# Performance work log

Hardware: AMD Instinct MI355X
Metric: run time of the kernel (lower is better)

The kernel has to match this reference:

```python
import jax, jax.numpy as jnp
import numpy as np

B, C, H, W = 8, 128, 64, 64  # dim = in_channels = 128, N = H*W = 4096
TEMP = float(C) ** 0.5


def _proj(x, w, b):
    # 1x1 conv: [B,C,H,W] x [D,C] -> [B,D,H,W]
    return jnp.einsum('bchw,dc->bdhw', x, w) + b[None, :, None, None]


def setup_inputs() -> dict:
    key = jax.random.key(0)
    ks = jax.random.split(key, 6)
    std = 0.01
    x = jax.random.normal(ks[0], (B, C, H, W), dtype=jnp.float32)
    wq = jax.random.normal(ks[1], (C, C), dtype=jnp.float32) * std
    wk = jax.random.normal(ks[2], (C, C), dtype=jnp.float32) * std
    wv = jax.random.normal(ks[3], (C, C), dtype=jnp.float32) * std
    wo = jax.random.normal(ks[4], (C, C), dtype=jnp.float32) * std
    zeros = jnp.zeros((C,), dtype=jnp.float32)
    return {"x": x, "wq": wq, "bq": zeros, "wk": wk, "bk": zeros,
            "wv": wv, "bv": zeros, "wo": wo, "bo": zeros}


def reference(x, wq, bq, wk, bk, wv, bv, wo, bo):
    n, c, h, w = x.shape
    N = h * w
    q = _proj(x, wq, bq).reshape(n, c, N)          # [B, D, N]
    k = _proj(x, wk, bk).reshape(n, c, N)          # [B, D, N]
    v = _proj(x, wv, bv).reshape(n, c, N)          # [B, D, N]
    # attn[b, i, j] = sum_d q[b,d,i] * k[b,d,j] / temp
    attn = jnp.einsum('bdi,bdj->bij', q, k) / TEMP  # [B, N, N]
    attn = jax.nn.softmax(attn, axis=-1)
    # y[b, d, i] = sum_j attn[b,i,j] * v[b,d,j]
    y = jnp.einsum('bij,bdj->bdi', attn, v).reshape(n, c, h, w)
    y = _proj(y, wo, bo)                            # conv_out
    return x + y                                    # identity residual
```

## Files before the change

kernel.cpp:

```cpp
#include <hip/hip_runtime.h>


typedef float  f32x4  __attribute__((ext_vector_type(4)));
typedef float  f32x16 __attribute__((ext_vector_type(16)));
typedef short  s16x8  __attribute__((ext_vector_type(8)));
typedef short  s16x4  __attribute__((ext_vector_type(4)));
typedef unsigned uint4v __attribute__((ext_vector_type(4)));

#define MFMA16(A, Bb, Cc) __builtin_amdgcn_mfma_f32_16x16x32_bf16(A, Bb, Cc, 0, 0, 0)
#define MFMA32(A, Bb, Cc) __builtin_amdgcn_mfma_f32_32x32x16_bf16(A, Bb, Cc, 0, 0, 0)

#define BATCH 8
#define DIM   128
#define NN    4096
#define NSPLIT 2
#define JCHUNK (NN / NSPLIT)
#define NT    (JCHUNK / 64)
#define Q_SCALE 0.12751649736784776f

#if __has_builtin(__builtin_amdgcn_exp2f)
#define EXP2(x) __builtin_amdgcn_exp2f(x)
#else
#define EXP2(x) exp2f(x)
#endif

__device__ __forceinline__ unsigned short f2bf(float f) {
  union { float f; unsigned u; } v; v.f = f;
  unsigned r = v.u + 0x7FFFu + ((v.u >> 16) & 1u);
  return (unsigned short)(r >> 16);
}
__device__ __forceinline__ float bf2f(unsigned short h) {
  union { unsigned u; float f; } v; v.u = ((unsigned)h) << 16;
  return v.f;
}
__device__ __forceinline__ s16x8 cvt8(const float* src) {
  float4 a = *(const float4*)src;
  float4 b = *(const float4*)(src + 4);
  s16x8 f;
  f[0] = (short)f2bf(a.x); f[1] = (short)f2bf(a.y);
  f[2] = (short)f2bf(a.z); f[3] = (short)f2bf(a.w);
  f[4] = (short)f2bf(b.x); f[5] = (short)f2bf(b.y);
  f[6] = (short)f2bf(b.z); f[7] = (short)f2bf(b.w);
  return f;
}

__global__ __launch_bounds__(256, 3) void qkv_kernel(
    const float* __restrict__ x,
    const float* __restrict__ wq, const float* __restrict__ wk,
    const float* __restrict__ wv,
    const float* __restrict__ bq, const float* __restrict__ bk,
    const float* __restrict__ bv,
    unsigned short* __restrict__ qt,
    unsigned short* __restrict__ kt,
    unsigned short* __restrict__ vv) {
  __shared__ unsigned short xs16[DIM * 72];
  __shared__ unsigned short wls[DIM * 136];
  const int b = blockIdx.y;
  const int i0 = blockIdx.x * 64;
  const int z = blockIdx.z;
  const int tid = threadIdx.x;

  const float* wsrc = (z == 0) ? wq : (z == 1) ? wk : wv;
  const float* bias = (z == 0) ? bq : (z == 1) ? bk : bv;
  const float sc = (z == 0) ? Q_SCALE : 1.0f;

  const int wr = tid >> 4, wc = tid & 15;
#pragma unroll
  for (int it = 0; it < 8; it++) {
    const int row = it * 16 + wr;
    *(s16x8*)(&wls[row * 136 + wc * 8]) = cvt8(wsrc + row * DIM + wc * 8);
  }
  for (int idx = tid; idx < 1024; idx += 256) {
    int c = idx >> 3, i8 = idx & 7;
    *(s16x8*)(&xs16[c * 72 + i8 * 8]) =
        cvt8(x + ((size_t)(b * DIM + c)) * NN + i0 + i8 * 8);
  }
  __syncthreads();

  const int w = tid >> 6, lane = tid & 63, quad = lane >> 4, l15 = lane & 15;
  const int iloc = w * 16 + l15;
  const int i = i0 + iloc;

  s16x8 bfrag[4];
#pragma unroll
  for (int ch = 0; ch < 4; ch++) {
    s16x8 f;
#pragma unroll
    for (int jj = 0; jj < 8; jj++) {
      int c = ch * 32 + quad * 8 + jj;
      f[jj] = (short)xs16[c * 72 + iloc];
    }
    bfrag[ch] = f;
  }

  for (int t = 0; t < 8; t++) {
    const int dl = t * 16;
    f32x4 acc = {0.f, 0.f, 0.f, 0.f};
#pragma unroll
    for (int ch = 0; ch < 4; ch++) {
      s16x8 af = *(const s16x8*)(&wls[(dl + l15) * 136 + ch * 32 + quad * 8]);
      acc = MFMA16(af, bfrag[ch], acc);
    }
    if (z < 2) {
      unsigned short* dstb = (z == 0) ? qt : kt;
      s16x4 o;
#pragma unroll
      for (int r = 0; r < 4; r++) {
        int d = dl + quad * 4 + r;
        o[r] = (short)f2bf((acc[r] + bias[d]) * sc);
      }
      *(s16x4*)(dstb + ((size_t)b * NN + i) * DIM + dl + quad * 4) = o;
    } else {
#pragma unroll
      for (int r = 0; r < 4; r++) {
        int d = dl + quad * 4 + r;
        vv[((size_t)b * DIM + d) * NN + i] = f2bf(acc[r] + bias[d]);
      }
    }
  }
}

__global__ __launch_bounds__(256, 2) void attn_kernel(
    const unsigned short* __restrict__ qt,
    const unsigned short* __restrict__ kt,
    const unsigned short* __restrict__ vv,
    unsigned short* __restrict__ o_part,
    float* __restrict__ l_part) {
  __shared__ unsigned short sh[32768];
  const int b = blockIdx.y;
  const int i0 = blockIdx.x * 128;
  const int split = blockIdx.z;
  const int jbase = split * JCHUNK;
  const int tid = threadIdx.x;
  const int w = tid >> 6, lane = tid & 63;
  const int l31 = lane & 31, h = lane >> 5;

  const unsigned short* kb = kt + (size_t)b * NN * DIM;
  const unsigned short* vb = vv + (size_t)b * DIM * NN;

  s16x8 qfrag[8];
  {
    const unsigned short* qrow =
        qt + ((size_t)b * NN + i0 + w * 32 + l31) * DIM + h * 8;
#pragma unroll
    for (int kc = 0; kc < 8; kc++)
      qfrag[kc] = *(const s16x8*)(qrow + kc * 16);
  }

  f32x16 acc[4];
#pragma unroll
  for (int mt = 0; mt < 4; mt++)
#pragma unroll
    for (int e = 0; e < 16; e++) acc[mt][e] = 0.f;
  float l_acc = 0.f;

  const int kr = tid >> 4, kc_ = tid & 15;
  const int vr = tid >> 3, vc = tid & 7;
  const int vch0 = (vc & 1) ? (vc - 1) : vc;
  const int vch1 = (vc & 1) ? vc : (vc + 1);
  const int vpos = (vc & 1) * 4;

  s16x8 kpre[4], vpre[4];

#pragma unroll
  for (int it = 0; it < 4; it++) {
    kpre[it] = *(const s16x8*)(kb + (size_t)(jbase + it * 16 + kr) * DIM + kc_ * 8);
    vpre[it] = *(const s16x8*)(vb + (size_t)(it * 32 + vr) * NN + jbase + vc * 8);
  }
#pragma unroll
  for (int it = 0; it < 4; it++) {
    const int r = it * 16 + kr;
    *(s16x8*)(sh + (((r << 4) + (kc_ ^ (r & 15))) << 3)) = kpre[it];
    const int r2 = it * 32 + vr;
    union { s16x8 v8; s16x4 v4[2]; } sp; sp.v8 = vpre[it];
    *(s16x4*)(sh + 8192 + (((r2 << 3) + (vch0 ^ (r2 & 7))) << 3) + vpos) = sp.v4[0];
    *(s16x4*)(sh + 8192 + (((r2 << 3) + (vch1 ^ (r2 & 7))) << 3) + vpos) = sp.v4[1];
  }
#pragma unroll
  for (int it = 0; it < 4; it++) {
    kpre[it] = *(const s16x8*)(kb + (size_t)(jbase + 64 + it * 16 + kr) * DIM + kc_ * 8);
    vpre[it] = *(const s16x8*)(vb + (size_t)(it * 32 + vr) * NN + jbase + 64 + vc * 8);
  }

  for (int t = 0; t < NT; t++) {
    __syncthreads();

    if (t + 1 < NT) {
      unsigned short* wb2 = sh + ((~t & 1) << 14);
#pragma unroll
      for (int it = 0; it < 4; it++) {
        const int r = it * 16 + kr;
        *(s16x8*)(wb2 + (((r << 4) + (kc_ ^ (r & 15))) << 3)) = kpre[it];
        const int r2 = it * 32 + vr;
        union { s16x8 v8; s16x4 v4[2]; } sp; sp.v8 = vpre[it];
        *(s16x4*)(wb2 + 8192 + (((r2 << 3) + (vch0 ^ (r2 & 7))) << 3) + vpos) = sp.v4[0];
        *(s16x4*)(wb2 + 8192 + (((r2 << 3) + (vch1 ^ (r2 & 7))) << 3) + vpos) = sp.v4[1];
      }
    }

    if (t + 2 < NT) {
      const int jn = jbase + (t + 2) * 64;
#pragma unroll
      for (int it = 0; it < 4; it++) {
        kpre[it] = *(const s16x8*)(kb + (size_t)(jn + it * 16 + kr) * DIM + kc_ * 8);
        vpre[it] = *(const s16x8*)(vb + (size_t)(it * 32 + vr) * NN + jn + vc * 8);
      }
    }

    const unsigned short* rK = sh + ((t & 1) << 14);
    const unsigned short* rV = rK + 8192;

#pragma unroll
    for (int jt = 0; jt < 2; jt++) {
      f32x16 S;
#pragma unroll
      for (int e = 0; e < 16; e++) S[e] = 0.f;
      const int j = jt * 32 + l31;
      __builtin_amdgcn_s_setprio(1);
#pragma unroll
      for (int kc = 0; kc < 8; kc++) {
        s16x8 kf = *(const s16x8*)(rK + (((j << 4) + ((2 * kc + h) ^ (j & 15))) << 3));
        S = MFMA32(kf, qfrag[kc], S);
      }
      __builtin_amdgcn_s_setprio(0);
      unsigned pk[8];
#pragma unroll
      for (int p = 0; p < 8; p++) {
        float e0 = EXP2(S[2 * p]), e1 = EXP2(S[2 * p + 1]);
        l_acc += e0 + e1;
        union { float f; unsigned u; } u0, u1; u0.f = e0; u1.f = e1;
        pk[p] = __builtin_amdgcn_perm(u1.u, u0.u, 0x07060302u);
      }
      __builtin_amdgcn_s_setprio(1);
#pragma unroll
      for (int bl = 0; bl < 2; bl++) {
        union { uint4v u; s16x8 v; } pu;
        pu.u[0] = pk[4 * bl + 0]; pu.u[1] = pk[4 * bl + 1];
        pu.u[2] = pk[4 * bl + 2]; pu.u[3] = pk[4 * bl + 3];
        const s16x8 pf = pu.v;
        const int c0 = (jt * 2 + bl) * 2 + h;
#pragma unroll
        for (int mt = 0; mt < 4; mt++) {
          const int d = mt * 32 + l31;
          s16x8 vf = *(const s16x8*)(rV + (((d << 3) + (c0 ^ (d & 7))) << 3));
          acc[mt] = MFMA32(vf, pf, acc[mt]);
        }
      }
      __builtin_amdgcn_s_setprio(0);
    }
  }

  const float l_tot = l_acc + __shfl_xor(l_acc, 32, 64);

  __syncthreads();
  unsigned short* ep = sh + w * 4096;
#pragma unroll
  for (int mt = 0; mt < 4; mt++)
#pragma unroll
    for (int reg = 0; reg < 16; reg++) {
      int d = mt * 32 + (reg & 3) + 8 * (reg >> 2) + 4 * h;
      int dc = d >> 3;
      ep[(l31 << 7) + ((dc ^ (l31 & 15)) << 3) + (d & 7)] = f2bf(acc[mt][reg]);
    }
  __syncthreads();
#pragma unroll
  for (int it = 0; it < 8; it++) {
    int qr = it * 4 + (lane >> 4), cr = lane & 15;
    s16x8 v = *(const s16x8*)(ep + (qr << 7) + ((cr ^ (qr & 15)) << 3));
    *(s16x8*)(o_part + (((size_t)split * BATCH + b) * NN + i0 + w * 32 + qr) * DIM +
              cr * 8) = v;
  }
  if (lane < 32)
    l_part[((size_t)split * BATCH + b) * NN + i0 + w * 32 + lane] = l_tot;
}

__global__ __launch_bounds__(256, 3) void outp_kernel(
    const float* __restrict__ x,
    const float* __restrict__ wo,
    const float* __restrict__ bo,
    const unsigned short* __restrict__ o_part,
    const float* __restrict__ l_part,
    float* __restrict__ out) {
  __shared__ unsigned short ytile[64 * 136];
  __shared__ unsigned short wls[DIM * 136];
  __shared__ float invl[64];
  const int b = blockIdx.y;
  const int i0 = blockIdx.x * 64;
  const int tid = threadIdx.x;
  const int ir = tid >> 4, g = tid & 15;

  s16x8 ov[4][2];
#pragma unroll
  for (int k = 0; k < 4; k++)
#pragma unroll
    for (int s = 0; s < NSPLIT; s++)
      ov[k][s] = *(const s16x8*)(o_part +
          (((size_t)s * BATCH + b) * NN + i0 + k * 16 + ir) * DIM + g * 8);

  const int wr = tid >> 4, wc = tid & 15;
#pragma unroll
  for (int it = 0; it < 8; it++) {
    const int row = it * 16 + wr;
    *(s16x8*)(&wls[row * 136 + wc * 8]) = cvt8(wo + row * DIM + wc * 8);
  }

  if (tid < 64) {
    float l = 0.f;
#pragma unroll
    for (int s = 0; s < NSPLIT; s++)
      l += l_part[((size_t)s * BATCH + b) * NN + i0 + tid];
    invl[tid] = 1.0f / l;
  }
  __syncthreads();

#pragma unroll
  for (int k = 0; k < 4; k++) {
    const int i = k * 16 + ir;
    const float inv = invl[i];
    s16x8 f;
#pragma unroll
    for (int jj = 0; jj < 8; jj++) {
      float o = bf2f((unsigned short)ov[k][0][jj]) + bf2f((unsigned short)ov[k][1][jj]);
      f[jj] = (short)f2bf(o * inv);
    }
    *(s16x8*)(&ytile[i * 136 + g * 8]) = f;
  }
  __syncthreads();

  const int w = tid >> 6, lane = tid & 63, quad = lane >> 4, l15 = lane & 15;
  const int i = i0 + w * 16 + l15;

  s16x8 bfrag[4];
#pragma unroll
  for (int ch = 0; ch < 4; ch++)
    bfrag[ch] = *(const s16x8*)(&ytile[(w * 16 + l15) * 136 + ch * 32 + quad * 8]);

  for (int t = 0; t < 8; t++) {
    f32x4 acc = {0.f, 0.f, 0.f, 0.f};
#pragma unroll
    for (int ch = 0; ch < 4; ch++) {
      s16x8 af = *(const s16x8*)(&wls[(t * 16 + l15) * 136 + ch * 32 + quad * 8]);
      acc = MFMA16(af, bfrag[ch], acc);
    }
#pragma unroll
    for (int r = 0; r < 4; r++) {
      int d = t * 16 + quad * 4 + r;
      size_t idx = ((size_t)b * DIM + d) * NN + i;
      out[idx] = x[idx] + acc[r] + bo[d];
    }
  }
}

extern "C" void kernel_launch(void* const* d_in, const int* in_sizes, int n_in,
                              void* d_out, int out_size, void* d_ws, size_t ws_size,
                              hipStream_t stream) {
  const float* x  = (const float*)d_in[0];
  const float* wq = (const float*)d_in[1];
  const float* bq = (const float*)d_in[2];
  const float* wk = (const float*)d_in[3];
  const float* bk = (const float*)d_in[4];
  const float* wv = (const float*)d_in[5];
  const float* bv = (const float*)d_in[6];
  const float* wo = (const float*)d_in[7];
  const float* bo = (const float*)d_in[8];
  float* out = (float*)d_out;

  unsigned short* ws  = (unsigned short*)d_ws;
  unsigned short* qt  = ws;
  unsigned short* kt  = qt + (size_t)BATCH * NN * DIM;
  unsigned short* vv  = kt + (size_t)BATCH * NN * DIM;
  unsigned short* o_part = vv + (size_t)BATCH * NN * DIM;
  float* l_part = (float*)(o_part + (size_t)NSPLIT * BATCH * NN * DIM);

  hipLaunchKernelGGL(qkv_kernel, dim3(64, 8, 3), dim3(256), 0, stream,
                     x, wq, wk, wv, bq, bk, bv, qt, kt, vv);
  hipLaunchKernelGGL(attn_kernel, dim3(32, 8, NSPLIT), dim3(256), 0, stream,
                     qt, kt, vv, o_part, l_part);
  hipLaunchKernelGGL(outp_kernel, dim3(64, 8), dim3(256), 0, stream,
                     x, wo, bo, o_part, l_part, out);
}
```

Baseline: 178.9 us.

## Split attention KV range four ways with smaller 32-column tiles for occupancy

The attention kernel is templated on the number of key splits and launches four splits when the workspace is large enough, falling back to two otherwise. The per-iteration key/value tile shrinks from 64 to 32 columns, which halves shared memory and raises launch bounds to four blocks per CU; the V-tile swizzle is adjusted to the narrower layout. The goal is more resident waves and more blocks to fill the GPU. The cost is twice as many partial outputs written and then reduced in the output kernel, plus more barriers per key processed.

```diff
diff --git a/kernel.cpp b/kernel.cpp
--- a/kernel.cpp
+++ b/kernel.cpp
@@ -13,9 +13,6 @@
 #define BATCH 8
 #define DIM   128
 #define NN    4096
-#define NSPLIT 2
-#define JCHUNK (NN / NSPLIT)
-#define NT    (JCHUNK / 64)
 #define Q_SCALE 0.12751649736784776f
 
 #if __has_builtin(__builtin_amdgcn_exp2f)
@@ -120,17 +117,20 @@
   }
 }
 
-__global__ __launch_bounds__(256, 2) void attn_kernel(
+template <int NS>
+__global__ __launch_bounds__(256, 4) void attn_kernel(
     const unsigned short* __restrict__ qt,
     const unsigned short* __restrict__ kt,
     const unsigned short* __restrict__ vv,
     unsigned short* __restrict__ o_part,
     float* __restrict__ l_part) {
-  __shared__ unsigned short sh[32768];
+  constexpr int JC  = NN / NS;
+  constexpr int NTI = JC / 32;
+  __shared__ unsigned short sh[16384];
   const int b = blockIdx.y;
   const int i0 = blockIdx.x * 128;
   const int split = blockIdx.z;
-  const int jbase = split * JCHUNK;
+  const int jbase = split * JC;
   const int tid = threadIdx.x;
   const int w = tid >> 6, lane = tid & 63;
   const int l31 = lane & 31, h = lane >> 5;
@@ -155,99 +155,99 @@
   float l_acc = 0.f;
 
   const int kr = tid >> 4, kc_ = tid & 15;
-  const int vr = tid >> 3, vc = tid & 7;
+  const int vr = tid >> 2, vc = tid & 3;
   const int vch0 = (vc & 1) ? (vc - 1) : vc;
   const int vch1 = (vc & 1) ? vc : (vc + 1);
   const int vpos = (vc & 1) * 4;
 
-  s16x8 kpre[4], vpre[4];
-
-#pragma unroll
-  for (int it = 0; it < 4; it++) {
+  s16x8 kpre[2], vpre[2];
+
+#pragma unroll
+  for (int it = 0; it < 2; it++) {
     kpre[it] = *(const s16x8*)(kb + (size_t)(jbase + it * 16 + kr) * DIM + kc_ * 8);
-    vpre[it] = *(const s16x8*)(vb + (size_t)(it * 32 + vr) * NN + jbase + vc * 8);
-  }
-#pragma unroll
-  for (int it = 0; it < 4; it++) {
+    vpre[it] = *(const s16x8*)(vb + (size_t)(it * 64 + vr) * NN + jbase + vc * 8);
+  }
+#pragma unroll
+  for (int it = 0; it < 2; it++) {
     const int r = it * 16 + kr;
     *(s16x8*)(sh + (((r << 4) + (kc_ ^ (r & 15))) << 3)) = kpre[it];
-    const int r2 = it * 32 + vr;
+    const int r2 = it * 64 + vr;
+    const int rx = (r2 & 3) ^ ((r2 >> 2) & 3);
     union { s16x8 v8; s16x4 v4[2]; } sp; sp.v8 = vpre[it];
-    *(s16x4*)(sh + 8192 + (((r2 << 3) + (vch0 ^ (r2 & 7))) << 3) + vpos) = sp.v4[0];
-    *(s16x4*)(sh + 8192 + (((r2 << 3) + (vch1 ^ (r2 & 7))) << 3) + vpos) = sp.v4[1];
-  }
-#pragma unroll
-  for (int it = 0; it < 4; it++) {
-    kpre[it] = *(const s16x8*)(kb + (size_t)(jbase + 64 + it * 16 + kr) * DIM + kc_ * 8);
-    vpre[it] = *(const s16x8*)(vb + (size_t)(it * 32 + vr) * NN + jbase + 64 + vc * 8);
-  }
-
-  for (int t = 0; t < NT; t++) {
+    *(s16x4*)(sh + 4096 + (((r2 << 2) + (vch0 ^ rx)) << 3) + vpos) = sp.v4[0];
+    *(s16x4*)(sh + 4096 + (((r2 << 2) + (vch1 ^ rx)) << 3) + vpos) = sp.v4[1];
+  }
+#pragma unroll
+  for (int it = 0; it < 2; it++) {
+    kpre[it] = *(const s16x8*)(kb + (size_t)(jbase + 32 + it * 16 + kr) * DIM + kc_ * 8);
+    vpre[it] = *(const s16x8*)(vb + (size_t)(it * 64 + vr) * NN + jbase + 32 + vc * 8);
+  }
+
+  for (int t = 0; t < NTI; t++) {
     __syncthreads();
 
-    if (t + 1 < NT) {
-      unsigned short* wb2 = sh + ((~t & 1) << 14);
-#pragma unroll
-      for (int it = 0; it < 4; it++) {
+    if (t + 1 < NTI) {
+      unsigned short* wb2 = sh + ((~t & 1) << 13);
+#pragma unroll
+      for (int it = 0; it < 2; it++) {
         const int r = it * 16 + kr;
         *(s16x8*)(wb2 + (((r << 4) + (kc_ ^ (r & 15))) << 3)) = kpre[it];
-        const int r2 = it * 32 + vr;
+        const int r2 = it * 64 + vr;
+        const int rx = (r2 & 3) ^ ((r2 >> 2) & 3);
         union { s16x8 v8; s16x4 v4[2]; } sp; sp.v8 = vpre[it];
-        *(s16x4*)(wb2 + 8192 + (((r2 << 3) + (vch0 ^ (r2 & 7))) << 3) + vpos) = sp.v4[0];
-        *(s16x4*)(wb2 + 8192 + (((r2 << 3) + (vch1 ^ (r2 & 7))) << 3) + vpos) = sp.v4[1];
-      }
-    }
-
-    if (t + 2 < NT) {
-      const int jn = jbase + (t + 2) * 64;
-#pragma unroll
-      for (int it = 0; it < 4; it++) {
+        *(s16x4*)(wb2 + 4096 + (((r2 << 2) + (vch0 ^ rx)) << 3) + vpos) = sp.v4[0];
+        *(s16x4*)(wb2 + 4096 + (((r2 << 2) + (vch1 ^ rx)) << 3) + vpos) = sp.v4[1];
+      }
+    }
+
+    if (t + 2 < NTI) {
+      const int jn = jbase + (t + 2) * 32;
+#pragma unroll
+      for (int it = 0; it < 2; it++) {
         kpre[it] = *(const s16x8*)(kb + (size_t)(jn + it * 16 + kr) * DIM + kc_ * 8);
-        vpre[it] = *(const s16x8*)(vb + (size_t)(it * 32 + vr) * NN + jn + vc * 8);
-      }
-    }
-
-    const unsigned short* rK = sh + ((t & 1) << 14);
-    const unsigned short* rV = rK + 8192;
-
-#pragma unroll
-    for (int jt = 0; jt < 2; jt++) {
-      f32x16 S;
-#pragma unroll
-      for (int e = 0; e < 16; e++) S[e] = 0.f;
-      const int j = jt * 32 + l31;
-      __builtin_amdgcn_s_setprio(1);
-#pragma unroll
-      for (int kc = 0; kc < 8; kc++) {
-        s16x8 kf = *(const s16x8*)(rK + (((j << 4) + ((2 * kc + h) ^ (j & 15))) << 3));
-        S = MFMA32(kf, qfrag[kc], S);
-      }
-      __builtin_amdgcn_s_setprio(0);
-      unsigned pk[8];
-#pragma unroll
-      for (int p = 0; p < 8; p++) {
-        float e0 = EXP2(S[2 * p]), e1 = EXP2(S[2 * p + 1]);
-        l_acc += e0 + e1;
-        union { float f; unsigned u; } u0, u1; u0.f = e0; u1.f = e1;
-        pk[p] = __builtin_amdgcn_perm(u1.u, u0.u, 0x07060302u);
-      }
-      __builtin_amdgcn_s_setprio(1);
-#pragma unroll
-      for (int bl = 0; bl < 2; bl++) {
-        union { uint4v u; s16x8 v; } pu;
-        pu.u[0] = pk[4 * bl + 0]; pu.u[1] = pk[4 * bl + 1];
-        pu.u[2] = pk[4 * bl + 2]; pu.u[3] = pk[4 * bl + 3];
-        const s16x8 pf = pu.v;
-        const int c0 = (jt * 2 + bl) * 2 + h;
-#pragma unroll
-        for (int mt = 0; mt < 4; mt++) {
-          const int d = mt * 32 + l31;
-          s16x8 vf = *(const s16x8*)(rV + (((d << 3) + (c0 ^ (d & 7))) << 3));
-          acc[mt] = MFMA32(vf, pf, acc[mt]);
-        }
-      }
-      __builtin_amdgcn_s_setprio(0);
-    }
+        vpre[it] = *(const s16x8*)(vb + (size_t)(it * 64 + vr) * NN + jn + vc * 8);
+      }
+    }
+
+    const unsigned short* rK = sh + ((t & 1) << 13);
+    const unsigned short* rV = rK + 4096;
+
+    f32x16 S;
+#pragma unroll
+    for (int e = 0; e < 16; e++) S[e] = 0.f;
+    const int j = l31;
+    __builtin_amdgcn_s_setprio(1);
+#pragma unroll
+    for (int kc = 0; kc < 8; kc++) {
+      s16x8 kf = *(const s16x8*)(rK + (((j << 4) + ((2 * kc + h) ^ (j & 15))) << 3));
+      S = MFMA32(kf, qfrag[kc], S);
+    }
+    __builtin_amdgcn_s_setprio(0);
+    unsigned pk[8];
+#pragma unroll
+    for (int p = 0; p < 8; p++) {
+      float e0 = EXP2(S[2 * p]), e1 = EXP2(S[2 * p + 1]);
+      l_acc += e0 + e1;
+      union { float f; unsigned u; } u0, u1; u0.f = e0; u1.f = e1;
+      pk[p] = __builtin_amdgcn_perm(u1.u, u0.u, 0x07060302u);
+    }
+    __builtin_amdgcn_s_setprio(1);
+#pragma unroll
+    for (int bl = 0; bl < 2; bl++) {
+      union { uint4v u; s16x8 v; } pu;
+      pu.u[0] = pk[4 * bl + 0]; pu.u[1] = pk[4 * bl + 1];
+      pu.u[2] = pk[4 * bl + 2]; pu.u[3] = pk[4 * bl + 3];
+      const s16x8 pf = pu.v;
+      const int c0 = bl * 2 + h;
+#pragma unroll
+      for (int mt = 0; mt < 4; mt++) {
+        const int d = mt * 32 + l31;
+        const int dx = (d & 3) ^ ((d >> 2) & 3);
+        s16x8 vf = *(const s16x8*)(rV + (((d << 2) + (c0 ^ dx)) << 3));
+        acc[mt] = MFMA32(vf, pf, acc[mt]);
+      }
+    }
+    __builtin_amdgcn_s_setprio(0);
   }
 
   const float l_tot = l_acc + __shfl_xor(l_acc, 32, 64);
@@ -274,6 +274,7 @@
     l_part[((size_t)split * BATCH + b) * NN + i0 + w * 32 + lane] = l_tot;
 }
 
+template <int NS>
 __global__ __launch_bounds__(256, 3) void outp_kernel(
     const float* __restrict__ x,
     const float* __restrict__ wo,
@@ -289,11 +290,11 @@
   const int tid = threadIdx.x;
   const int ir = tid >> 4, g = tid & 15;
 
-  s16x8 ov[4][2];
+  s16x8 ov[4][NS];
 #pragma unroll
   for (int k = 0; k < 4; k++)
 #pragma unroll
-    for (int s = 0; s < NSPLIT; s++)
+    for (int s = 0; s < NS; s++)
       ov[k][s] = *(const s16x8*)(o_part +
           (((size_t)s * BATCH + b) * NN + i0 + k * 16 + ir) * DIM + g * 8);
 
@@ -307,7 +308,7 @@
   if (tid < 64) {
     float l = 0.f;
 #pragma unroll
-    for (int s = 0; s < NSPLIT; s++)
+    for (int s = 0; s < NS; s++)
       l += l_part[((size_t)s * BATCH + b) * NN + i0 + tid];
     invl[tid] = 1.0f / l;
   }
@@ -320,7 +321,9 @@
     s16x8 f;
 #pragma unroll
     for (int jj = 0; jj < 8; jj++) {
-      float o = bf2f((unsigned short)ov[k][0][jj]) + bf2f((unsigned short)ov[k][1][jj]);
+      float o = 0.f;
+#pragma unroll
+      for (int s = 0; s < NS; s++) o += bf2f((unsigned short)ov[k][s][jj]);
       f[jj] = (short)f2bf(o * inv);
     }
     *(s16x8*)(&ytile[i * 136 + g * 8]) = f;
@@ -370,12 +373,24 @@
   unsigned short* kt  = qt + (size_t)BATCH * NN * DIM;
   unsigned short* vv  = kt + (size_t)BATCH * NN * DIM;
   unsigned short* o_part = vv + (size_t)BATCH * NN * DIM;
-  float* l_part = (float*)(o_part + (size_t)NSPLIT * BATCH * NN * DIM);
+
+  const size_t base = (size_t)3 * BATCH * NN * DIM * 2;
+  const size_t need4 = base + (size_t)4 * BATCH * NN * DIM * 2 + (size_t)4 * BATCH * NN * 4;
 
   hipLaunchKernelGGL(qkv_kernel, dim3(64, 8, 3), dim3(256), 0, stream,
                      x, wq, wk, wv, bq, bk, bv, qt, kt, vv);
-  hipLaunchKernelGGL(attn_kernel, dim3(32, 8, NSPLIT), dim3(256), 0, stream,
-                     qt, kt, vv, o_part, l_part);
-  hipLaunchKernelGGL(outp_kernel, dim3(64, 8), dim3(256), 0, stream,
-                     x, wo, bo, o_part, l_part, out);
-}
+
+  if (ws_size >= need4) {
+    float* l_part = (float*)(o_part + (size_t)4 * BATCH * NN * DIM);
+    hipLaunchKernelGGL((attn_kernel<4>), dim3(32, 8, 4), dim3(256), 0, stream,
+                       qt, kt, vv, o_part, l_part);
+    hipLaunchKernelGGL((outp_kernel<4>), dim3(64, 8), dim3(256), 0, stream,
+                       x, wo, bo, o_part, l_part, out);
+  } else {
+    float* l_part = (float*)(o_part + (size_t)2 * BATCH * NN * DIM);
+    hipLaunchKernelGGL((attn_kernel<2>), dim3(32, 8, 2), dim3(256), 0, stream,
+                       qt, kt, vv, o_part, l_part);
+    hipLaunchKernelGGL((outp_kernel<2>), dim3(64, 8), dim3(256), 0, stream,
+                       x, wo, bo, o_part, l_part, out);
+  }
+}
```

Result: slower. 311.9 us (+74.3%).
